# Kernel tuning notes

Measured on AMD Instinct MI355X. Metric: run time of the kernel, lower is better.

The kernel has to match this reference:

```python
import jax, jax.numpy as jnp
import numpy as np

NEG = -10000.0  # fp16-safe mask value, as in the torch module


def prelu(x, a):
    # nn.PReLU() default: single learnable slope shared across channels
    return jnp.where(x >= 0, x, a * x)


def setup_inputs() -> dict:
    key = jax.random.key(0)
    ks = jax.random.split(key, 9)
    B, L, D = 2048, 200, 128
    H1, H2 = 256, 128
    query = jax.random.normal(ks[0], (B, D), dtype=jnp.float32)
    keys = jax.random.normal(ks[1], (B, L, D), dtype=jnp.float32)
    mask = jax.random.randint(ks[2], (B, L), 0, 2, dtype=jnp.int32)
    s1 = 1.0 / np.sqrt(4 * D)
    s2 = 1.0 / np.sqrt(H1)
    s3 = 1.0 / np.sqrt(H2)
    W1 = jax.random.uniform(ks[3], (H1, 4 * D), minval=-s1, maxval=s1, dtype=jnp.float32)
    b1 = jax.random.uniform(ks[4], (H1,), minval=-s1, maxval=s1, dtype=jnp.float32)
    W2 = jax.random.uniform(ks[5], (H2, H1), minval=-s2, maxval=s2, dtype=jnp.float32)
    b2 = jax.random.uniform(ks[6], (H2,), minval=-s2, maxval=s2, dtype=jnp.float32)
    W3 = jax.random.uniform(ks[7], (1, H2), minval=-s3, maxval=s3, dtype=jnp.float32)
    b3 = jax.random.uniform(ks[8], (1,), minval=-s3, maxval=s3, dtype=jnp.float32)
    a1 = jnp.asarray(0.25, dtype=jnp.float32)  # PReLU init
    a2 = jnp.asarray(0.25, dtype=jnp.float32)
    return {"query": query, "keys": keys, "mask": mask,
            "W1": W1, "b1": b1, "a1": a1, "W2": W2, "b2": b2, "a2": a2,
            "W3": W3, "b3": b3}


def reference(query, keys, mask, W1, b1, a1, W2, b2, a2, W3, b3):
    B, L, D = keys.shape
    q = jnp.broadcast_to(query[:, None, :], (B, L, D))
    # [B, L, 4D] concat feature (query, key, diff, product)
    att_in = jnp.concatenate([q, keys, q - keys, q * keys], axis=-1)
    h = prelu(jnp.einsum('blf,hf->blh', att_in, W1) + b1, a1)
    h = prelu(jnp.einsum('blh,gh->blg', h, W2) + b2, a2)
    scores = (jnp.einsum('blg,og->blo', h, W3) + b3)[..., 0]  # [B, L]
    scores = jnp.where(mask == 0, NEG, scores)
    w = jax.nn.softmax(scores, axis=-1)
    w = jnp.where(mask == 0, 0.0, w)
    # weighted sum over history -> user interest [B, D]
    return jnp.einsum('bl,bld->bd', w, keys)
```

## Files before the change

### kernel.cpp

```cpp
#include <hip/hip_runtime.h>
#include <cstdint>

#define NEGV (-10000.0f)

typedef short bf16x8 __attribute__((ext_vector_type(8)));
typedef float f32x4 __attribute__((ext_vector_type(4)));

__device__ __forceinline__ short f2bf(float f) {
  union { float f; uint32_t u; } v; v.f = f;
  uint32_t u = v.u + 0x7fffu + ((v.u >> 16) & 1u);
  return (short)(u >> 16);
}
__device__ __forceinline__ float b2f(short s) {
  union { uint32_t u; float f; } v; v.u = ((uint32_t)(uint16_t)s) << 16;
  return v.f;
}

__global__ void prep_weights(const float* __restrict__ W1, const float* __restrict__ W2,
                             short* __restrict__ Wk, short* __restrict__ Wd,
                             short* __restrict__ W2b) {
  int idx = blockIdx.x * 256 + threadIdx.x;
  if (idx < 32768) {
    int h = idx >> 7, d = idx & 127;
    Wk[idx] = f2bf(W1[h * 512 + 128 + d] - W1[h * 512 + 256 + d]);
  } else if (idx < 65536) {
    int i = idx - 32768;
    int h = i >> 7, d = i & 127;
    Wd[i] = f2bf(W1[h * 512 + 384 + d]);
  } else {
    int i = idx - 65536;
    W2b[i] = f2bf(W2[i]);
  }
}

__global__ void prep_u(const float* __restrict__ query, const float* __restrict__ W1,
                       const float* __restrict__ b1, float* __restrict__ U) {
  __shared__ float q8[8][128];
  int tid = threadIdx.x;
  int b0 = blockIdx.x * 8;
  for (int i = tid; i < 1024; i += 256)
    q8[i >> 7][i & 127] = query[(size_t)(b0 + (i >> 7)) * 128 + (i & 127)];
  __syncthreads();
  int h = tid;
  const float4* w0 = (const float4*)(W1 + (size_t)h * 512);
  const float4* w1 = (const float4*)(W1 + (size_t)h * 512 + 256);
  float acc[8];
  float bb = b1[h];
#pragma unroll
  for (int i = 0; i < 8; ++i) acc[i] = bb;
  for (int d4 = 0; d4 < 32; ++d4) {
    float4 wa = w0[d4], wb = w1[d4];
    float wv0 = wa.x + wb.x, wv1 = wa.y + wb.y, wv2 = wa.z + wb.z, wv3 = wa.w + wb.w;
#pragma unroll
    for (int i = 0; i < 8; ++i) {
      float4 qv = ((const float4*)q8[i])[d4];
      acc[i] += wv0 * qv.x + wv1 * qv.y + wv2 * qv.z + wv3 * qv.w;
    }
  }
#pragma unroll
  for (int i = 0; i < 8; ++i) U[(size_t)(b0 + i) * 256 + h] = acc[i];
}

__global__ __launch_bounds__(256, 2) void din_main(
    const float* __restrict__ query, const float* __restrict__ keys,
    const int* __restrict__ mask,
    const float* __restrict__ b2p, const float* __restrict__ a1p,
    const float* __restrict__ a2p, const float* __restrict__ W3,
    const float* __restrict__ b3p,
    const float* __restrict__ U, const short* __restrict__ Wk,
    const short* __restrict__ Wd, const short* __restrict__ W2b,
    float* __restrict__ out) {
  __shared__ short Kl[208 * 128];
  __shared__ short H1[16 * 256];
  __shared__ float scores[208];
  __shared__ float wl[208];
  __shared__ float red[8];
  __shared__ float opart[128];

  const int tid = threadIdx.x;
  const int b = blockIdx.x;
  const int lane = tid & 63, wid = tid >> 6;
  const int lr = lane & 15;
  const int lg = lane >> 4;

  const float a1 = a1p[0], a2 = a2p[0], b3 = b3p[0];

  for (int it = tid; it < 208 * 16; it += 256) {
    int l = it >> 4, c8 = it & 15;
    bf16x8 v;
    if (l < 200) {
      const float4* kp = (const float4*)(keys + ((size_t)b * 200 + l) * 128 + c8 * 8);
      float4 x0 = kp[0], x1 = kp[1];
      v[0] = f2bf(x0.x); v[1] = f2bf(x0.y); v[2] = f2bf(x0.z); v[3] = f2bf(x0.w);
      v[4] = f2bf(x1.x); v[5] = f2bf(x1.y); v[6] = f2bf(x1.z); v[7] = f2bf(x1.w);
    } else {
#pragma unroll
      for (int j = 0; j < 8; ++j) v[j] = 0;
    }
    *(bf16x8*)(&Kl[l * 128 + ((c8 * 8) ^ ((l & 7) << 3))]) = v;
  }
  if (tid < 208) scores[tid] = b3;

  bf16x8 mf[4][4];
  float uval[4];
  {
    const float* qrow = query + (size_t)b * 128;
#pragma unroll
    for (int nt = 0; nt < 4; ++nt) {
      int h = wid * 64 + nt * 16 + lr;
      uval[nt] = U[(size_t)b * 256 + h];
#pragma unroll
      for (int ks = 0; ks < 4; ++ks) {
        int d0 = ks * 32 + lg * 8;
        bf16x8 wk = *(const bf16x8*)(Wk + h * 128 + d0);
        bf16x8 wd = *(const bf16x8*)(Wd + h * 128 + d0);
        float4 q0 = *(const float4*)(qrow + d0);
        float4 q1 = *(const float4*)(qrow + d0 + 4);
        float qv[8] = {q0.x, q0.y, q0.z, q0.w, q1.x, q1.y, q1.z, q1.w};
        bf16x8 r;
#pragma unroll
        for (int j = 0; j < 8; ++j) r[j] = f2bf(b2f(wk[j]) + b2f(wd[j]) * qv[j]);
        mf[nt][ks] = r;
      }
    }
  }
  bf16x8 w2f[2][8];
  float b2v[2], w3v[2];
#pragma unroll
  for (int nt = 0; nt < 2; ++nt) {
    int g = wid * 32 + nt * 16 + lr;
    b2v[nt] = b2p[g];
    w3v[nt] = W3[g];
#pragma unroll
    for (int ks = 0; ks < 8; ++ks)
      w2f[nt][ks] = *(const bf16x8*)(W2b + g * 256 + ks * 32 + lg * 8);
  }
  __syncthreads();

  for (int mt = 0; mt < 13; ++mt) {
    const int al = mt * 16 + lr;
    bf16x8 af[4];
#pragma unroll
    for (int ks = 0; ks < 4; ++ks)
      af[ks] = *(const bf16x8*)(&Kl[al * 128 + ((ks * 32 + lg * 8) ^ ((al & 7) << 3))]);

    f32x4 acc1[4];
#pragma unroll
    for (int nt = 0; nt < 4; ++nt)
#pragma unroll
      for (int r = 0; r < 4; ++r) acc1[nt][r] = 0.f;
#pragma unroll
    for (int ks = 0; ks < 4; ++ks)
#pragma unroll
      for (int nt = 0; nt < 4; ++nt)
        acc1[nt] = __builtin_amdgcn_mfma_f32_16x16x32_bf16(af[ks], mf[nt][ks], acc1[nt], 0, 0, 0);

#pragma unroll
    for (int nt = 0; nt < 4; ++nt) {
      int col = wid * 64 + nt * 16 + lr;
#pragma unroll
      for (int r = 0; r < 4; ++r) {
        int row = lg * 4 + r;
        float v = acc1[nt][r] + uval[nt];
        v = (v >= 0.f) ? v : a1 * v;
        H1[row * 256 + (col ^ ((row & 7) << 3))] = f2bf(v);
      }
    }
    __syncthreads();

    f32x4 acc2[2];
#pragma unroll
    for (int nt = 0; nt < 2; ++nt)
#pragma unroll
      for (int r = 0; r < 4; ++r) acc2[nt][r] = 0.f;
#pragma unroll
    for (int ks = 0; ks < 8; ++ks) {
      bf16x8 a2f = *(const bf16x8*)(&H1[lr * 256 + ((ks * 32 + lg * 8) ^ ((lr & 7) << 3))]);
      acc2[0] = __builtin_amdgcn_mfma_f32_16x16x32_bf16(a2f, w2f[0][ks], acc2[0], 0, 0, 0);
      acc2[1] = __builtin_amdgcn_mfma_f32_16x16x32_bf16(a2f, w2f[1][ks], acc2[1], 0, 0, 0);
    }

    float sp[4];
#pragma unroll
    for (int r = 0; r < 4; ++r) {
      float s = 0.f;
#pragma unroll
      for (int nt = 0; nt < 2; ++nt) {
        float v = acc2[nt][r] + b2v[nt];
        v = (v >= 0.f) ? v : a2 * v;
        s += v * w3v[nt];
      }
      sp[r] = s;
    }
#pragma unroll
    for (int m = 1; m < 16; m <<= 1)
#pragma unroll
      for (int r = 0; r < 4; ++r) sp[r] += __shfl_xor(sp[r], m);
    if (lr == 0) {
#pragma unroll
      for (int r = 0; r < 4; ++r) atomicAdd(&scores[mt * 16 + lg * 4 + r], sp[r]);
    }
    __syncthreads();
  }

  float val = NEGV;
  int mk = 0;
  if (tid < 200) {
    mk = mask[(size_t)b * 200 + tid];
    float sc = scores[tid];
    val = mk ? sc : NEGV;
  }
  float m = val;
#pragma unroll
  for (int off = 1; off < 64; off <<= 1) m = fmaxf(m, __shfl_xor(m, off));
  if ((tid & 63) == 0) red[tid >> 6] = m;
  __syncthreads();
  float smax = fmaxf(fmaxf(red[0], red[1]), fmaxf(red[2], red[3]));
  float p = (tid < 200 && mk) ? __expf(val - smax) : 0.f;
  float s = p;
#pragma unroll
  for (int off = 1; off < 64; off <<= 1) s += __shfl_xor(s, off);
  if ((tid & 63) == 0) red[4 + (tid >> 6)] = s;
  __syncthreads();
  float ssum = red[4] + red[5] + red[6] + red[7];
  float winv = (ssum > 0.f) ? 1.f / ssum : 0.f;
  if (tid < 208) wl[tid] = (tid < 200) ? p * winv : 0.f;
  __syncthreads();

  const int d = tid & 127, half = tid >> 7;
  float acc = 0.f;
  for (int l = half; l < 200; l += 2) {
    float wv = wl[l];
    if (wv != 0.f) {
      short kv = Kl[l * 128 + (d ^ ((l & 7) << 3))];
      acc += wv * b2f(kv);
    }
  }
  if (half) opart[d] = acc;
  __syncthreads();
  if (!half) out[(size_t)b * 128 + d] = acc + opart[d];
}

extern "C" void kernel_launch(void* const* d_in, const int* in_sizes, int n_in,
                              void* d_out, int out_size, void* d_ws, size_t ws_size,
                              hipStream_t stream) {
  const float* query = (const float*)d_in[0];
  const float* keys  = (const float*)d_in[1];
  const int*   maskp = (const int*)d_in[2];
  const float* W1    = (const float*)d_in[3];
  const float* b1    = (const float*)d_in[4];
  const float* a1    = (const float*)d_in[5];
  const float* W2    = (const float*)d_in[6];
  const float* b2    = (const float*)d_in[7];
  const float* a2    = (const float*)d_in[8];
  const float* W3    = (const float*)d_in[9];
  const float* b3    = (const float*)d_in[10];
  float* out = (float*)d_out;

  float* U   = (float*)d_ws;
  short* Wk  = (short*)((char*)d_ws + 2097152);
  short* Wd  = Wk + 32768;
  short* W2b = Wd + 32768;

  prep_weights<<<384, 256, 0, stream>>>(W1, W2, Wk, Wd, W2b);
  prep_u<<<256, 256, 0, stream>>>(query, W1, b1, U);
  din_main<<<2048, 256, 0, stream>>>(query, keys, maskp, b2, a1, a2, W3, b3,
                                     U, Wk, Wd, W2b, out);
}
```

Measured before the change: 178.6 us.

## Double-buffer key chunks with 512-thread blocks and transposed MFMA layout

The main kernel now uses 512 threads (8 waves) and stages the keys into shared memory in 64-row chunks. The next chunk's global load is issued before the current chunk's MFMA work, so loads overlap compute, and all 200 rows no longer have to be staged upfront. The MFMA operands are swapped so H1 is written as packed bf16x4 and the score reduction needs fewer shuffles. The final weighted sum re-reads the keys from global memory in fp32 instead of from bf16 shared memory. This adds a second pass over the keys in global memory and raises LDS use per block, which may limit occupancy.

```diff
diff --git a/kernel.cpp b/kernel.cpp
--- a/kernel.cpp
+++ b/kernel.cpp
@@ -1,9 +1,11 @@
 #include <hip/hip_runtime.h>
+#include <hip/hip_bf16.h>
 #include <cstdint>
 
 #define NEGV (-10000.0f)
 
 typedef short bf16x8 __attribute__((ext_vector_type(8)));
+typedef short bf16x4 __attribute__((ext_vector_type(4)));
 typedef float f32x4 __attribute__((ext_vector_type(4)));
 
 __device__ __forceinline__ short f2bf(float f) {
@@ -14,6 +16,12 @@
 __device__ __forceinline__ float b2f(short s) {
   union { uint32_t u; float f; } v; v.u = ((uint32_t)(uint16_t)s) << 16;
   return v.f;
+}
+__device__ __forceinline__ uint32_t pk2(float lo, float hi) {
+  union { __hip_bfloat162 h2; uint32_t u; } cv;
+  cv.h2.x = __float2bfloat16(lo);
+  cv.h2.y = __float2bfloat16(hi);
+  return cv.u;
 }
 
 __global__ void prep_weights(const float* __restrict__ W1, const float* __restrict__ W2,
@@ -61,7 +69,7 @@
   for (int i = 0; i < 8; ++i) U[(size_t)(b0 + i) * 256 + h] = acc[i];
 }
 
-__global__ __launch_bounds__(256, 2) void din_main(
+__global__ __launch_bounds__(512, 4) void din_main(
     const float* __restrict__ query, const float* __restrict__ keys,
     const int* __restrict__ mask,
     const float* __restrict__ b2p, const float* __restrict__ a1p,
@@ -70,45 +78,33 @@
     const float* __restrict__ U, const short* __restrict__ Wk,
     const short* __restrict__ Wd, const short* __restrict__ W2b,
     float* __restrict__ out) {
-  __shared__ short Kl[208 * 128];
-  __shared__ short H1[16 * 256];
+  __shared__ short Kp[2][64 * 128];
+  __shared__ short H1[64 * 256];
   __shared__ float scores[208];
   __shared__ float wl[208];
-  __shared__ float red[8];
-  __shared__ float opart[128];
+  __shared__ float Ul[256];
+  __shared__ float b2l[128];
+  __shared__ float w3l[128];
+  __shared__ float red[16];
+  __shared__ float opart[16 * 128];
 
   const int tid = threadIdx.x;
   const int b = blockIdx.x;
   const int lane = tid & 63, wid = tid >> 6;
-  const int lr = lane & 15;
-  const int lg = lane >> 4;
+  const int lr = lane & 15, lg = lane >> 4;
 
   const float a1 = a1p[0], a2 = a2p[0], b3 = b3p[0];
 
-  for (int it = tid; it < 208 * 16; it += 256) {
-    int l = it >> 4, c8 = it & 15;
-    bf16x8 v;
-    if (l < 200) {
-      const float4* kp = (const float4*)(keys + ((size_t)b * 200 + l) * 128 + c8 * 8);
-      float4 x0 = kp[0], x1 = kp[1];
-      v[0] = f2bf(x0.x); v[1] = f2bf(x0.y); v[2] = f2bf(x0.z); v[3] = f2bf(x0.w);
-      v[4] = f2bf(x1.x); v[5] = f2bf(x1.y); v[6] = f2bf(x1.z); v[7] = f2bf(x1.w);
-    } else {
-#pragma unroll
-      for (int j = 0; j < 8; ++j) v[j] = 0;
-    }
-    *(bf16x8*)(&Kl[l * 128 + ((c8 * 8) ^ ((l & 7) << 3))]) = v;
-  }
+  if (tid < 256) Ul[tid] = U[(size_t)b * 256 + tid];
+  if (tid < 128) { b2l[tid] = b2p[tid]; w3l[tid] = W3[tid]; }
   if (tid < 208) scores[tid] = b3;
 
-  bf16x8 mf[4][4];
-  float uval[4];
+  bf16x8 mf[2][4];
   {
     const float* qrow = query + (size_t)b * 128;
 #pragma unroll
-    for (int nt = 0; nt < 4; ++nt) {
-      int h = wid * 64 + nt * 16 + lr;
-      uval[nt] = U[(size_t)b * 256 + h];
+    for (int nt = 0; nt < 2; ++nt) {
+      int h = wid * 32 + nt * 16 + lr;
 #pragma unroll
       for (int ks = 0; ks < 4; ++ks) {
         int d0 = ks * 32 + lg * 8;
@@ -117,88 +113,120 @@
         float4 q0 = *(const float4*)(qrow + d0);
         float4 q1 = *(const float4*)(qrow + d0 + 4);
         float qv[8] = {q0.x, q0.y, q0.z, q0.w, q1.x, q1.y, q1.z, q1.w};
-        bf16x8 r;
-#pragma unroll
-        for (int j = 0; j < 8; ++j) r[j] = f2bf(b2f(wk[j]) + b2f(wd[j]) * qv[j]);
-        mf[nt][ks] = r;
-      }
-    }
-  }
-  bf16x8 w2f[2][8];
-  float b2v[2], w3v[2];
-#pragma unroll
-  for (int nt = 0; nt < 2; ++nt) {
-    int g = wid * 32 + nt * 16 + lr;
-    b2v[nt] = b2p[g];
-    w3v[nt] = W3[g];
+        float mv[8];
+#pragma unroll
+        for (int j = 0; j < 8; ++j) mv[j] = b2f(wk[j]) + b2f(wd[j]) * qv[j];
+        union { bf16x8 v; uint32_t u[4]; } mm;
+#pragma unroll
+        for (int j = 0; j < 4; ++j) mm.u[j] = pk2(mv[2 * j], mv[2 * j + 1]);
+        mf[nt][ks] = mm.v;
+      }
+    }
+  }
+  bf16x8 w2f[8];
+  {
+    int g = wid * 16 + lr;
 #pragma unroll
     for (int ks = 0; ks < 8; ++ks)
-      w2f[nt][ks] = *(const bf16x8*)(W2b + g * 256 + ks * 32 + lg * 8);
-  }
-  __syncthreads();
-
-  for (int mt = 0; mt < 13; ++mt) {
-    const int al = mt * 16 + lr;
-    bf16x8 af[4];
-#pragma unroll
-    for (int ks = 0; ks < 4; ++ks)
-      af[ks] = *(const bf16x8*)(&Kl[al * 128 + ((ks * 32 + lg * 8) ^ ((al & 7) << 3))]);
-
-    f32x4 acc1[4];
-#pragma unroll
-    for (int nt = 0; nt < 4; ++nt)
-#pragma unroll
-      for (int r = 0; r < 4; ++r) acc1[nt][r] = 0.f;
-#pragma unroll
-    for (int ks = 0; ks < 4; ++ks)
-#pragma unroll
-      for (int nt = 0; nt < 4; ++nt)
-        acc1[nt] = __builtin_amdgcn_mfma_f32_16x16x32_bf16(af[ks], mf[nt][ks], acc1[nt], 0, 0, 0);
-
-#pragma unroll
-    for (int nt = 0; nt < 4; ++nt) {
-      int col = wid * 64 + nt * 16 + lr;
+      w2f[ks] = *(const bf16x8*)(W2b + g * 256 + ks * 32 + lg * 8);
+  }
+
+  const int srow = tid >> 3, sc = (tid & 7) * 16;
+  {
+    const float4* kp4 = (const float4*)(keys + ((size_t)b * 200 + srow) * 128 + sc);
+    float4 s0 = kp4[0], s1 = kp4[1], s2 = kp4[2], s3 = kp4[3];
+    union { bf16x8 v; uint32_t u[4]; } w0, w1;
+    w0.u[0] = pk2(s0.x, s0.y); w0.u[1] = pk2(s0.z, s0.w);
+    w0.u[2] = pk2(s1.x, s1.y); w0.u[3] = pk2(s1.z, s1.w);
+    w1.u[0] = pk2(s2.x, s2.y); w1.u[1] = pk2(s2.z, s2.w);
+    w1.u[2] = pk2(s3.x, s3.y); w1.u[3] = pk2(s3.z, s3.w);
+    int sw = (srow & 7) << 3;
+    *(bf16x8*)(&Kp[0][srow * 128 + (sc ^ sw)]) = w0.v;
+    *(bf16x8*)(&Kp[0][srow * 128 + ((sc + 8) ^ sw)]) = w1.v;
+  }
+  __syncthreads();
+
+  for (int p = 0; p < 4; ++p) {
+    const int buf = p & 1;
+    const int nsub = (p < 3) ? 4 : 1;
+
+    float4 st0, st1, st2, st3;
+    bool svalid = false;
+    if (p < 3) {
+      int nrow = (p + 1 < 3) ? 64 : 16;
+      svalid = srow < nrow;
+      int sl = (p + 1) * 64 + srow;
+      st0 = st1 = st2 = st3 = make_float4(0.f, 0.f, 0.f, 0.f);
+      if (svalid && sl < 200) {
+        const float4* kp4 = (const float4*)(keys + ((size_t)b * 200 + sl) * 128 + sc);
+        st0 = kp4[0]; st1 = kp4[1]; st2 = kp4[2]; st3 = kp4[3];
+      }
+    }
+
+    for (int sub = 0; sub < nsub; ++sub) {
+      const int l = sub * 16 + lr;
+      const int sw = (lr & 7) << 3;
+      bf16x8 kf[4];
+#pragma unroll
+      for (int ks = 0; ks < 4; ++ks)
+        kf[ks] = *(const bf16x8*)(&Kp[buf][l * 128 + ((ks * 32 + lg * 8) ^ sw)]);
+      f32x4 acc[2];
+#pragma unroll
+      for (int nt = 0; nt < 2; ++nt)
+#pragma unroll
+        for (int r = 0; r < 4; ++r) acc[nt][r] = Ul[wid * 32 + nt * 16 + lg * 4 + r];
+#pragma unroll
+      for (int ks = 0; ks < 4; ++ks)
+#pragma unroll
+        for (int nt = 0; nt < 2; ++nt)
+          acc[nt] = __builtin_amdgcn_mfma_f32_16x16x32_bf16(mf[nt][ks], kf[ks], acc[nt], 0, 0, 0);
+#pragma unroll
+      for (int nt = 0; nt < 2; ++nt) {
+        float v0 = acc[nt][0], v1 = acc[nt][1], v2 = acc[nt][2], v3 = acc[nt][3];
+        v0 = (v0 >= 0.f) ? v0 : a1 * v0;
+        v1 = (v1 >= 0.f) ? v1 : a1 * v1;
+        v2 = (v2 >= 0.f) ? v2 : a1 * v2;
+        v3 = (v3 >= 0.f) ? v3 : a1 * v3;
+        union { bf16x4 v; uint32_t u[2]; } hh;
+        hh.u[0] = pk2(v0, v1); hh.u[1] = pk2(v2, v3);
+        int h0 = wid * 32 + nt * 16 + lg * 4;
+        *(bf16x4*)(&H1[l * 256 + (h0 ^ sw)]) = hh.v;
+      }
+    }
+
+    if (svalid) {
+      union { bf16x8 v; uint32_t u[4]; } w0, w1;
+      w0.u[0] = pk2(st0.x, st0.y); w0.u[1] = pk2(st0.z, st0.w);
+      w0.u[2] = pk2(st1.x, st1.y); w0.u[3] = pk2(st1.z, st1.w);
+      w1.u[0] = pk2(st2.x, st2.y); w1.u[1] = pk2(st2.z, st2.w);
+      w1.u[2] = pk2(st3.x, st3.y); w1.u[3] = pk2(st3.z, st3.w);
+      int sw2 = (srow & 7) << 3;
+      *(bf16x8*)(&Kp[buf ^ 1][srow * 128 + (sc ^ sw2)]) = w0.v;
+      *(bf16x8*)(&Kp[buf ^ 1][srow * 128 + ((sc + 8) ^ sw2)]) = w1.v;
+    }
+    __syncthreads();
+
+    for (int sub = 0; sub < nsub; ++sub) {
+      const int hrow = sub * 16 + lr;
+      const int sw = (lr & 7) << 3;
+      f32x4 acc2;
+#pragma unroll
+      for (int r = 0; r < 4; ++r) acc2[r] = b2l[wid * 16 + lg * 4 + r];
+#pragma unroll
+      for (int ks = 0; ks < 8; ++ks) {
+        bf16x8 hf = *(const bf16x8*)(&H1[hrow * 256 + ((ks * 32 + lg * 8) ^ sw)]);
+        acc2 = __builtin_amdgcn_mfma_f32_16x16x32_bf16(w2f[ks], hf, acc2, 0, 0, 0);
+      }
+      float s = 0.f;
 #pragma unroll
       for (int r = 0; r < 4; ++r) {
-        int row = lg * 4 + r;
-        float v = acc1[nt][r] + uval[nt];
-        v = (v >= 0.f) ? v : a1 * v;
-        H1[row * 256 + (col ^ ((row & 7) << 3))] = f2bf(v);
-      }
-    }
-    __syncthreads();
-
-    f32x4 acc2[2];
-#pragma unroll
-    for (int nt = 0; nt < 2; ++nt)
-#pragma unroll
-      for (int r = 0; r < 4; ++r) acc2[nt][r] = 0.f;
-#pragma unroll
-    for (int ks = 0; ks < 8; ++ks) {
-      bf16x8 a2f = *(const bf16x8*)(&H1[lr * 256 + ((ks * 32 + lg * 8) ^ ((lr & 7) << 3))]);
-      acc2[0] = __builtin_amdgcn_mfma_f32_16x16x32_bf16(a2f, w2f[0][ks], acc2[0], 0, 0, 0);
-      acc2[1] = __builtin_amdgcn_mfma_f32_16x16x32_bf16(a2f, w2f[1][ks], acc2[1], 0, 0, 0);
-    }
-
-    float sp[4];
-#pragma unroll
-    for (int r = 0; r < 4; ++r) {
-      float s = 0.f;
-#pragma unroll
-      for (int nt = 0; nt < 2; ++nt) {
-        float v = acc2[nt][r] + b2v[nt];
+        float v = acc2[r];
         v = (v >= 0.f) ? v : a2 * v;
-        s += v * w3v[nt];
-      }
-      sp[r] = s;
-    }
-#pragma unroll
-    for (int m = 1; m < 16; m <<= 1)
-#pragma unroll
-      for (int r = 0; r < 4; ++r) sp[r] += __shfl_xor(sp[r], m);
-    if (lr == 0) {
-#pragma unroll
-      for (int r = 0; r < 4; ++r) atomicAdd(&scores[mt * 16 + lg * 4 + r], sp[r]);
+        s += v * w3l[wid * 16 + lg * 4 + r];
+      }
+      s += __shfl_xor(s, 16);
+      s += __shfl_xor(s, 32);
+      if (lg == 0) atomicAdd(&scores[p * 64 + sub * 16 + lr], s);
     }
     __syncthreads();
   }
@@ -207,38 +235,48 @@
   int mk = 0;
   if (tid < 200) {
     mk = mask[(size_t)b * 200 + tid];
-    float sc = scores[tid];
-    val = mk ? sc : NEGV;
+    val = mk ? scores[tid] : NEGV;
   }
   float m = val;
 #pragma unroll
   for (int off = 1; off < 64; off <<= 1) m = fmaxf(m, __shfl_xor(m, off));
-  if ((tid & 63) == 0) red[tid >> 6] = m;
-  __syncthreads();
-  float smax = fmaxf(fmaxf(red[0], red[1]), fmaxf(red[2], red[3]));
-  float p = (tid < 200 && mk) ? __expf(val - smax) : 0.f;
-  float s = p;
+  if (lane == 0) red[wid] = m;
+  __syncthreads();
+  float smax = red[0];
+#pragma unroll
+  for (int i = 1; i < 8; ++i) smax = fmaxf(smax, red[i]);
+  float pex = (tid < 200 && mk) ? __expf(val - smax) : 0.f;
+  float s = pex;
 #pragma unroll
   for (int off = 1; off < 64; off <<= 1) s += __shfl_xor(s, off);
-  if ((tid & 63) == 0) red[4 + (tid >> 6)] = s;
-  __syncthreads();
-  float ssum = red[4] + red[5] + red[6] + red[7];
+  if (lane == 0) red[8 + wid] = s;
+  __syncthreads();
+  float ssum = 0.f;
+#pragma unroll
+  for (int i = 0; i < 8; ++i) ssum += red[8 + i];
   float winv = (ssum > 0.f) ? 1.f / ssum : 0.f;
-  if (tid < 208) wl[tid] = (tid < 200) ? p * winv : 0.f;
-  __syncthreads();
-
-  const int d = tid & 127, half = tid >> 7;
-  float acc = 0.f;
-  for (int l = half; l < 200; l += 2) {
-    float wv = wl[l];
-    if (wv != 0.f) {
-      short kv = Kl[l * 128 + (d ^ ((l & 7) << 3))];
-      acc += wv * b2f(kv);
-    }
-  }
-  if (half) opart[d] = acc;
-  __syncthreads();
-  if (!half) out[(size_t)b * 128 + d] = acc + opart[d];
+  if (tid < 208) wl[tid] = (tid < 200) ? pex * winv : 0.f;
+  __syncthreads();
+
+  {
+    const int d4 = (tid & 31) << 2;
+    const int slice = tid >> 5;
+    float ax = 0.f, ay = 0.f, az = 0.f, aw = 0.f;
+    for (int l = slice; l < 200; l += 16) {
+      float wv = wl[l];
+      float4 kv = *(const float4*)(keys + ((size_t)b * 200 + l) * 128 + d4);
+      ax += wv * kv.x; ay += wv * kv.y; az += wv * kv.z; aw += wv * kv.w;
+    }
+    float4 r4 = make_float4(ax, ay, az, aw);
+    *(float4*)(&opart[slice * 128 + d4]) = r4;
+  }
+  __syncthreads();
+  if (tid < 128) {
+    float acc = 0.f;
+#pragma unroll
+    for (int i = 0; i < 16; ++i) acc += opart[i * 128 + tid];
+    out[(size_t)b * 128 + tid] = acc;
+  }
 }
 
 extern "C" void kernel_launch(void* const* d_in, const int* in_sizes, int n_in,
@@ -264,6 +302,6 @@
 
   prep_weights<<<384, 256, 0, stream>>>(W1, W2, Wk, Wd, W2b);
   prep_u<<<256, 256, 0, stream>>>(query, W1, b1, U);
-  din_main<<<2048, 256, 0, stream>>>(query, keys, maskp, b2, a1, a2, W3, b3,
+  din_main<<<2048, 512, 0, stream>>>(query, keys, maskp, b2, a1, a2, W3, b3,
                                      U, Wk, Wd, W2b, out);
 }
```

Result: slower. 415.7 us (+132.8%).
